# Performance work log

Hardware: AMD Instinct MI355X
Metric: run time of the kernel (lower is better)

The kernel has to match this reference:

```python
import jax, jax.numpy as jnp
import numpy as np
import math

CHANNELS = 1024
N_HEADS = 16
K_CHANNELS = CHANNELS // N_HEADS  # 64
ROPE_D = int(K_CHANNELS * 0.5)    # 32
B, T = 4, 2048


def apply_rope(x, d, base=10000.0):
    # x: [b, h, t, c]; rotate first d dims, pass the rest through
    t = x.shape[2]
    theta = 1.0 / (base ** (jnp.arange(0, d, 2, dtype=jnp.float32) / d))  # [d/2]
    idx_theta = jnp.arange(t, dtype=jnp.float32)[:, None] * theta[None, :]  # [t, d/2]
    idx_theta2 = jnp.concatenate([idx_theta, idx_theta], axis=-1)  # [t, d]
    cos = jnp.cos(idx_theta2)[None, None, :, :]
    sin = jnp.sin(idx_theta2)[None, None, :, :]
    x_rope, x_pass = x[..., :d], x[..., d:]
    d2 = d // 2
    neg_half = jnp.concatenate([-x_rope[..., d2:], x_rope[..., :d2]], axis=-1)
    x_rope = x_rope * cos + neg_half * sin
    return jnp.concatenate([x_rope, x_pass], axis=-1)


def setup_inputs() -> dict:
    key = jax.random.key(0)
    ks = jax.random.split(key, 12)
    xavier = math.sqrt(6.0 / (CHANNELS + CHANNELS))
    inp = {
        "x": jax.random.normal(ks[0], (B, CHANNELS, T), dtype=jnp.float32),
        "c": jax.random.normal(ks[1], (B, CHANNELS, T), dtype=jnp.float32),
        "attn_mask": jnp.ones((1, 1, T, T), dtype=jnp.int32),
        "wq": jax.random.uniform(ks[2], (CHANNELS, CHANNELS), jnp.float32, -xavier, xavier),
        "bq": jnp.zeros((CHANNELS,), jnp.float32),
        "wk": jax.random.uniform(ks[3], (CHANNELS, CHANNELS), jnp.float32, -xavier, xavier),
        "bk": jnp.zeros((CHANNELS,), jnp.float32),
        "wv": jax.random.uniform(ks[4], (CHANNELS, CHANNELS), jnp.float32, -xavier, xavier),
        "bv": jnp.zeros((CHANNELS,), jnp.float32),
        "wo": jax.random.normal(ks[5], (CHANNELS, CHANNELS), jnp.float32) * (1.0 / math.sqrt(CHANNELS)),
        "bo": jnp.zeros((CHANNELS,), jnp.float32),
    }
    return inp


def reference(x, c, attn_mask, wq, bq, wk, bk, wv, bv, wo, bo):
    b, _, t_t = x.shape
    t_s = c.shape[2]
    # Conv1d with kernel size 1 == per-timestep linear
    q = jnp.einsum('oi,bit->bot', wq, x) + bq[None, :, None]
    k = jnp.einsum('oi,bit->bot', wk, c) + bk[None, :, None]
    v = jnp.einsum('oi,bit->bot', wv, c) + bv[None, :, None]
    # b (h c) t -> b h t c
    def split_heads(z, t):
        return z.reshape(b, N_HEADS, K_CHANNELS, t).transpose(0, 1, 3, 2)
    q = split_heads(q, t_t)
    k = split_heads(k, t_s)
    v = split_heads(v, t_s)
    q = apply_rope(q, ROPE_D)
    k = apply_rope(k, ROPE_D)
    scores = jnp.einsum('bhqc,bhkc->bhqk', q, k) / math.sqrt(K_CHANNELS)
    scores = jnp.where(attn_mask == 0, jnp.float32(-10000.0), scores)
    p_attn = jax.nn.softmax(scores, axis=-1)
    out = jnp.einsum('bhqk,bhkc->bhqc', p_attn, v)
    # b h t c -> b h c t -> b (h c) t
    out = out.transpose(0, 1, 3, 2).reshape(b, CHANNELS, t_t)
    out = jnp.einsum('oi,bit->bot', wo, out) + bo[None, :, None]
    return out
```

## Files before the change

### kernel.cpp

```cpp
#include <hip/hip_runtime.h>
#include <stdint.h>

#define TT 2048
#define CC 1024
#define NHH 16
#define HD 64

using short8  = __attribute__((ext_vector_type(8))) short;
using short4v = __attribute__((ext_vector_type(4))) short;
using f32x4   = __attribute__((ext_vector_type(4))) float;
using ushort8 = __attribute__((ext_vector_type(8))) unsigned short;

typedef const __attribute__((address_space(1))) void* gptr_t;
typedef __attribute__((address_space(3))) void* lptr_t;

__device__ __forceinline__ unsigned short f2bf(float f){
  union { float f; unsigned int u; } v; v.f = f;
  unsigned int r = v.u + 0x7fffu + ((v.u >> 16) & 1u);
  return (unsigned short)(r >> 16);
}
__device__ __forceinline__ float bf2f(unsigned short u){
  union { unsigned int u; float f; } v; v.u = ((unsigned int)u) << 16;
  return v.f;
}
__device__ __forceinline__ uint32_t cvtpk_bf16(float lo, float hi){
  uint32_t r;
  asm("v_cvt_pk_bf16_f32 %0, %1, %2" : "=v"(r) : "v"(lo), "v"(hi));
  return r;
}
__device__ __forceinline__ float fexp2(float x){
#if __has_builtin(__builtin_amdgcn_exp2f)
  return __builtin_amdgcn_exp2f(x);
#else
  return exp2f(x);
#endif
}
__device__ __forceinline__ f32x4 mfma16x16x16bf16(short4v a, short4v b, f32x4 c){
#if __has_builtin(__builtin_amdgcn_mfma_f32_16x16x16bf16_1k)
  return __builtin_amdgcn_mfma_f32_16x16x16bf16_1k(a, b, c, 0, 0, 0);
#else
  asm("v_mfma_f32_16x16x16_bf16 %0, %1, %2, %0" : "+v"(c) : "v"(a), "v"(b));
  return c;
#endif
}

__global__ void wconv_kernel(const float* __restrict__ wq, const float* __restrict__ wk,
                             const float* __restrict__ wv, const float* __restrict__ wo,
                             unsigned short* __restrict__ W){
  int w = blockIdx.x >> 9;
  const float* s = (w==0)? wq : (w==1)? wk : (w==2)? wv : wo;
  size_t rem = ((size_t)(blockIdx.x & 511) * 256 + threadIdx.x) * 8;
  float4 a = *(const float4*)(s + rem);
  float4 b = *(const float4*)(s + rem + 4);
  ushort8 o;
  o[0]=f2bf(a.x); o[1]=f2bf(a.y); o[2]=f2bf(a.z); o[3]=f2bf(a.w);
  o[4]=f2bf(b.x); o[5]=f2bf(b.y); o[6]=f2bf(b.z); o[7]=f2bf(b.w);
  *(ushort8*)(W + (size_t)w*1048576 + rem) = o;
}

__global__ void tcast_kernel(const float* __restrict__ x, const float* __restrict__ c,
                             unsigned short* __restrict__ xT, unsigned short* __restrict__ cT){
  int z = blockIdx.z; int tensor = z >> 2; int b = z & 3;
  const float* src = (tensor ? c : x) + (size_t)b*CC*TT;
  unsigned short* dst = (tensor ? cT : xT) + (size_t)b*TT*CC;
  int t0 = blockIdx.x*64, c0 = blockIdx.y*64;
  __shared__ unsigned short ls[64][66];
  int tid = threadIdx.x;
  int r = tid >> 2, q = tid & 3;
  const float4* p = (const float4*)(src + (size_t)(c0+r)*TT + t0 + q*16);
  float4 vv[4]; vv[0]=p[0]; vv[1]=p[1]; vv[2]=p[2]; vv[3]=p[3];
  unsigned short* lp = &ls[r][q*16];
#pragma unroll
  for (int i=0;i<4;i++){
    lp[i*4+0]=f2bf(vv[i].x); lp[i*4+1]=f2bf(vv[i].y);
    lp[i*4+2]=f2bf(vv[i].z); lp[i*4+3]=f2bf(vv[i].w);
  }
  __syncthreads();
  unsigned short tmp[16] __attribute__((aligned(16)));
#pragma unroll
  for (int j=0;j<16;j++) tmp[j] = ls[q*16+j][r];
  unsigned short* dp = dst + (size_t)(t0+r)*CC + c0 + q*16;
  *(ushort8*)dp       = *(ushort8*)tmp;
  *(ushort8*)(dp + 8) = *(ushort8*)(tmp+8);
}

__device__ __forceinline__ void rope_write(
    const f32x4 (&acc)[4][4], const float* __restrict__ bias,
    unsigned short* __restrict__ dst,
    int b, int m0, int wr, int n0, int wc, int lane, float sc)
{
  int crow = (lane>>4)*4;
  int h = (m0 + wr) >> 6;
  size_t bh = (size_t)b*NHH + h;
  float th[4];
#pragma unroll
  for (int r=0;r<4;r++)
    th[r] = exp2f(-0.8304820237218405f * (float)(crow + r));
  float bv[4][4];
#pragma unroll
  for (int m=0;m<4;m++)
#pragma unroll
    for (int r=0;r<4;r++)
      bv[m][r] = bias[m0 + wr + m*16 + crow + r];
#pragma unroll
  for (int n=0;n<4;n++){
    int t = n0 + wc + n*16 + (lane&15);
    float tf = (float)t;
    float o_[4][4];
#pragma unroll
    for (int r=0;r<4;r++){
      float sn, cs;
      sincosf(tf * th[r], &sn, &cs);
      float v0 = acc[0][n][r] + bv[0][r];
      float v1 = acc[1][n][r] + bv[1][r];
      o_[0][r] = (v0*cs - v1*sn)*sc;
      o_[1][r] = (v1*cs + v0*sn)*sc;
      o_[2][r] = (acc[2][n][r] + bv[2][r])*sc;
      o_[3][r] = (acc[3][n][r] + bv[3][r])*sc;
    }
    unsigned short* dp = dst + (bh*TT + t)*HD + crow;
#pragma unroll
    for (int m=0;m<4;m++){
      uint2 pk;
      pk.x = cvtpk_bf16(o_[m][0], o_[m][1]);
      pk.y = cvtpk_bf16(o_[m][2], o_[m][3]);
      *(uint2*)(dp + m*16) = pk;
    }
  }
}

template<bool F32OUT>
__global__ __launch_bounds__(256) void gemm_kernel(
    const unsigned short* __restrict__ A,
    const unsigned short* __restrict__ Bm,
    const float* __restrict__ bias,
    void* __restrict__ outp)
{
  __shared__ unsigned short As[128*64];
  __shared__ unsigned short Bs[128*64];
  int b  = blockIdx.z;
  int m0 = blockIdx.x * 128;
  int n0 = blockIdx.y * 128;
  const unsigned short* Bb = Bm + (size_t)b*TT*CC;
  int tid = threadIdx.x;
  int lane = tid & 63, wave = tid >> 6;
  int wr = (wave>>1)*64, wc = (wave&1)*64;
  int srow = lane >> 3;
  int scolb = ((lane & 7) ^ srow) << 4;
  f32x4 acc[4][4] = {};
  for (int kt = 0; kt < 1024; kt += 64){
    __syncthreads();
#pragma unroll
    for (int i=0;i<4;i++){
      int ch = wave*4 + i;
      int row = ch*8 + srow;
      const char* g = (const char*)(A + (size_t)(m0+row)*1024 + kt) + scolb;
      __builtin_amdgcn_global_load_lds((gptr_t)g, (lptr_t)(As + ch*512), 16, 0, 0);
    }
#pragma unroll
    for (int i=0;i<4;i++){
      int ch = wave*4 + i;
      int row = ch*8 + srow;
      const char* g = (const char*)(Bb + (size_t)(n0+row)*1024 + kt) + scolb;
      __builtin_amdgcn_global_load_lds((gptr_t)g, (lptr_t)(Bs + ch*512), 16, 0, 0);
    }
    __syncthreads();
#pragma unroll
    for (int kk=0;kk<2;kk++){
      int kb = kk*64 + ((lane>>4)<<4);
      short8 af[4], bf[4];
#pragma unroll
      for (int m=0;m<4;m++){
        int row = wr + m*16 + (lane&15);
        af[m] = *(const short8*)((const char*)As + row*128 + (kb ^ ((row&7)<<4)));
      }
#pragma unroll
      for (int n=0;n<4;n++){
        int row = wc + n*16 + (lane&15);
        bf[n] = *(const short8*)((const char*)Bs + row*128 + (kb ^ ((row&7)<<4)));
      }
#pragma unroll
      for (int m=0;m<4;m++)
#pragma unroll
        for (int n=0;n<4;n++)
          acc[m][n] = __builtin_amdgcn_mfma_f32_16x16x32_bf16(af[m], bf[n], acc[m][n], 0, 0, 0);
    }
  }
  int crow = (lane>>4)*4;
#pragma unroll
  for (int m=0;m<4;m++){
#pragma unroll
    for (int r=0;r<4;r++){
      int o = m0 + wr + m*16 + crow + r;
      float bv = bias[o];
#pragma unroll
      for (int n=0;n<4;n++){
        int t = n0 + wc + n*16 + (lane&15);
        float v = acc[m][n][r] + bv;
        if (F32OUT) ((float*)outp)[(size_t)b*CC*TT + (size_t)o*TT + t] = v;
        else ((unsigned short*)outp)[(size_t)b*CC*TT + (size_t)o*TT + t] = f2bf(v);
      }
    }
  }
}

__global__ __launch_bounds__(256) void q_gemm_kernel(
    const unsigned short* __restrict__ A,
    const unsigned short* __restrict__ Bm,
    const float* __restrict__ bias,
    unsigned short* __restrict__ Qh)
{
  __shared__ unsigned short As[128*64];
  __shared__ unsigned short Bs[128*64];
  int b  = blockIdx.z;
  int m0 = blockIdx.x * 128;
  int n0 = blockIdx.y * 128;
  const unsigned short* Bb = Bm + (size_t)b*TT*CC;
  int tid = threadIdx.x;
  int lane = tid & 63, wave = tid >> 6;
  int wr = (wave>>1)*64, wc = (wave&1)*64;
  int srow = lane >> 3;
  int scolb = ((lane & 7) ^ srow) << 4;
  f32x4 acc[4][4] = {};
  for (int kt = 0; kt < 1024; kt += 64){
    __syncthreads();
#pragma unroll
    for (int i=0;i<4;i++){
      int ch = wave*4 + i;
      int row = ch*8 + srow;
      const char* g = (const char*)(A + (size_t)(m0+row)*1024 + kt) + scolb;
      __builtin_amdgcn_global_load_lds((gptr_t)g, (lptr_t)(As + ch*512), 16, 0, 0);
      const char* g2 = (const char*)(Bb + (size_t)(n0+row)*1024 + kt) + scolb;
      __builtin_amdgcn_global_load_lds((gptr_t)g2, (lptr_t)(Bs + ch*512), 16, 0, 0);
    }
    __syncthreads();
#pragma unroll
    for (int kk=0;kk<2;kk++){
      int kb = kk*64 + ((lane>>4)<<4);
      short8 af[4], bf[4];
#pragma unroll
      for (int m=0;m<4;m++){
        int row = wr + m*16 + (lane&15);
        af[m] = *(const short8*)((const char*)As + row*128 + (kb ^ ((row&7)<<4)));
      }
#pragma unroll
      for (int n=0;n<4;n++){
        int row = wc + n*16 + (lane&15);
        bf[n] = *(const short8*)((const char*)Bs + row*128 + (kb ^ ((row&7)<<4)));
      }
#pragma unroll
      for (int m=0;m<4;m++)
#pragma unroll
        for (int n=0;n<4;n++)
          acc[m][n] = __builtin_amdgcn_mfma_f32_16x16x32_bf16(af[m], bf[n], acc[m][n], 0, 0, 0);
    }
  }
  rope_write(acc, bias, Qh, b, m0, wr, n0, wc, lane, 0.18033688011112042f);
}

__global__ __launch_bounds__(256, 2) void kv_gemm_kernel(
    const unsigned short* __restrict__ Wk,
    const unsigned short* __restrict__ Wv,
    const unsigned short* __restrict__ Bm,
    const float* __restrict__ biask, const float* __restrict__ biasv,
    unsigned short* __restrict__ Kh, unsigned short* __restrict__ outV)
{
  __shared__ unsigned short AsK[128*64];
  __shared__ unsigned short AsV[128*64];
  __shared__ unsigned short Bs[128*64];
  int b  = blockIdx.z;
  int m0 = blockIdx.x * 128;
  int n0 = blockIdx.y * 128;
  const unsigned short* Bb = Bm + (size_t)b*TT*CC;
  int tid = threadIdx.x;
  int lane = tid & 63, wave = tid >> 6;
  int wr = (wave>>1)*64, wc = (wave&1)*64;
  int srow = lane >> 3;
  int scolb = ((lane & 7) ^ srow) << 4;
  f32x4 accK[4][4] = {};
  f32x4 accV[4][4] = {};
  for (int kt = 0; kt < 1024; kt += 64){
    __syncthreads();
#pragma unroll
    for (int i=0;i<4;i++){
      int ch = wave*4 + i;
      int row = ch*8 + srow;
      const char* gk = (const char*)(Wk + (size_t)(m0+row)*1024 + kt) + scolb;
      __builtin_amdgcn_global_load_lds((gptr_t)gk, (lptr_t)(AsK + ch*512), 16, 0, 0);
      const char* gv = (const char*)(Wv + (size_t)(m0+row)*1024 + kt) + scolb;
      __builtin_amdgcn_global_load_lds((gptr_t)gv, (lptr_t)(AsV + ch*512), 16, 0, 0);
      const char* gb = (const char*)(Bb + (size_t)(n0+row)*1024 + kt) + scolb;
      __builtin_amdgcn_global_load_lds((gptr_t)gb, (lptr_t)(Bs + ch*512), 16, 0, 0);
    }
    __syncthreads();
#pragma unroll
    for (int kk=0;kk<2;kk++){
      int kb = kk*64 + ((lane>>4)<<4);
      short8 bf[4];
#pragma unroll
      for (int n=0;n<4;n++){
        int row = wc + n*16 + (lane&15);
        bf[n] = *(const short8*)((const char*)Bs + row*128 + (kb ^ ((row&7)<<4)));
      }
#pragma unroll
      for (int m=0;m<4;m++){
        int row = wr + m*16 + (lane&15);
        int ro = row*128 + (kb ^ ((row&7)<<4));
        short8 afk = *(const short8*)((const char*)AsK + ro);
        short8 afv = *(const short8*)((const char*)AsV + ro);
#pragma unroll
        for (int n=0;n<4;n++){
          accK[m][n] = __builtin_amdgcn_mfma_f32_16x16x32_bf16(afk, bf[n], accK[m][n], 0, 0, 0);
          accV[m][n] = __builtin_amdgcn_mfma_f32_16x16x32_bf16(afv, bf[n], accV[m][n], 0, 0, 0);
        }
      }
    }
  }
  int crow = (lane>>4)*4;
#pragma unroll
  for (int m=0;m<4;m++){
#pragma unroll
    for (int r=0;r<4;r++){
      int o = m0 + wr + m*16 + crow + r;
      float bvv = biasv[o];
#pragma unroll
      for (int n=0;n<4;n++){
        int t = n0 + wc + n*16 + (lane&15);
        outV[(size_t)b*CC*TT + (size_t)o*TT + t] = f2bf(accV[m][n][r] + bvv);
      }
    }
  }
  rope_write(accK, biask, Kh, b, m0, wr, n0, wc, lane, 1.0f);
}

__global__ __launch_bounds__(256, 4) void attn_kernel(
    const unsigned short* __restrict__ Qh, const unsigned short* __restrict__ Kh,
    const unsigned short* __restrict__ Vn, unsigned short* __restrict__ AO)
{
  __shared__ unsigned short Ks[2][64*64];
  __shared__ unsigned short Vs[2][64*64];
  int Hf = blockIdx.x + (blockIdx.y << 4);
  int s8 = Hf >> 3;
  int bh = (Hf & 7) + ((s8 >> 4) << 3);
  int q0 = (s8 & 15) * 128;
  int b = bh >> 4, h = bh & 15;
  int tid = threadIdx.x, lane = tid & 63, wave = tid >> 6;
  const unsigned short* Qb = Qh + (size_t)bh*TT*HD;
  const unsigned short* Kb = Kh + (size_t)bh*TT*HD;
  const unsigned short* Vb = Vn + (size_t)b*CC*TT + (size_t)h*64*TT;
  int srow = lane >> 3, scolb = ((lane & 7) ^ srow) << 4;
  int g = lane >> 4;

  union { short4v s; uint32_t u[2]; } ones;
  ones.u[0] = ((lane & 15) == 0) ? 0x3F803F80u : 0u;
  ones.u[1] = ones.u[0];

  short8 qf[2][2];
#pragma unroll
  for (int n=0;n<2;n++)
#pragma unroll
    for (int kk=0;kk<2;kk++){
      int qrow = q0 + wave*32 + n*16 + (lane&15);
      qf[n][kk] = *(const short8*)((const char*)(Qb + (size_t)qrow*HD) + kk*64 + g*16);
    }

  f32x4 accO[4][2] = {};
  f32x4 accL[2] = {};

#pragma unroll
  for (int i=0;i<2;i++){
    int ch = wave*2 + i;
    int row = ch*8 + srow;
    const char* gk = (const char*)(Kb + (size_t)row*HD) + scolb;
    __builtin_amdgcn_global_load_lds((gptr_t)gk, (lptr_t)(Ks[0] + ch*512), 16, 0, 0);
    const char* gv = (const char*)(Vb + (size_t)row*TT) + scolb;
    __builtin_amdgcn_global_load_lds((gptr_t)gv, (lptr_t)(Vs[0] + ch*512), 16, 0, 0);
  }
  __syncthreads();

  const int NT = TT/64;
  for (int t=0; t<NT; ++t){
    int cur = t & 1;
    if (t+1 < NT){
      int kv0n = (t+1)*64;
#pragma unroll
      for (int i=0;i<2;i++){
        int ch = wave*2 + i;
        int row = ch*8 + srow;
        const char* gk = (const char*)(Kb + (size_t)(kv0n+row)*HD) + scolb;
        __builtin_amdgcn_global_load_lds((gptr_t)gk, (lptr_t)(Ks[cur^1] + ch*512), 16, 0, 0);
        const char* gv = (const char*)(Vb + (size_t)row*TT + kv0n) + scolb;
        __builtin_amdgcn_global_load_lds((gptr_t)gv, (lptr_t)(Vs[cur^1] + ch*512), 16, 0, 0);
      }
    }

    const char* KsC = (const char*)Ks[cur];
    f32x4 accS[4][2];
#pragma unroll
    for (int m=0;m<4;m++)
#pragma unroll
      for (int n=0;n<2;n++){
        accS[m][n][0]=accS[m][n][1]=accS[m][n][2]=accS[m][n][3]=-16.0f;
      }
    __builtin_amdgcn_s_setprio(1);
#pragma unroll
    for (int kk=0;kk<2;kk++){
      int kb = kk*64 + g*16;
      short8 kf[4];
#pragma unroll
      for (int m=0;m<4;m++){
        int row = m*16 + (lane&15);
        kf[m] = *(const short8*)(KsC + row*128 + (kb ^ ((row&7)<<4)));
      }
#pragma unroll
      for (int m=0;m<4;m++)
#pragma unroll
        for (int n=0;n<2;n++)
          accS[m][n] = __builtin_amdgcn_mfma_f32_16x16x32_bf16(kf[m], qf[n][kk], accS[m][n], 0, 0, 0);
    }
    __builtin_amdgcn_s_setprio(0);

#pragma unroll
    for (int n=0;n<2;n++)
#pragma unroll
      for (int m=0;m<4;m++)
#pragma unroll
        for (int r=0;r<4;r++)
          accS[m][n][r] = fexp2(accS[m][n][r]);

    union { short4v s; uint32_t u[2]; } pu[4][2];
#pragma unroll
    for (int m=0;m<4;m++)
#pragma unroll
      for (int n=0;n<2;n++){
        pu[m][n].u[0] = cvtpk_bf16(accS[m][n][0], accS[m][n][1]);
        pu[m][n].u[1] = cvtpk_bf16(accS[m][n][2], accS[m][n][3]);
      }
    const char* VsC = (const char*)Vs[cur];
    int r7 = lane & 7;
    int halfb = (g & 1) << 3;
    __builtin_amdgcn_s_setprio(1);
#pragma unroll
    for (int m=0;m<4;m++){
      int slot = m*2 + (g>>1);
      int coff = ((slot ^ r7) << 4) | halfb;
#pragma unroll
      for (int dt=0;dt<4;dt++){
        int row = dt*16 + (lane&15);
        short4v vf = *(const short4v*)(VsC + row*128 + coff);
#pragma unroll
        for (int n=0;n<2;n++)
          accO[dt][n] = mfma16x16x16bf16(vf, pu[m][n].s, accO[dt][n]);
      }
#pragma unroll
      for (int n=0;n<2;n++)
        accL[n] = mfma16x16x16bf16(ones.s, pu[m][n].s, accL[n]);
    }
    __builtin_amdgcn_s_setprio(0);

    __syncthreads();
  }

#pragma unroll
  for (int n=0;n<2;n++){
    int t = q0 + wave*32 + n*16 + (lane&15);
    float lsum = __shfl(accL[n][0], lane & 15);
    float rl = 1.0f / lsum;
#pragma unroll
    for (int m=0;m<4;m++){
      uint2 pk;
      pk.x = cvtpk_bf16(accO[m][n][0]*rl, accO[m][n][1]*rl);
      pk.y = cvtpk_bf16(accO[m][n][2]*rl, accO[m][n][3]*rl);
      *(uint2*)(AO + ((size_t)b*TT + t)*CC + h*64 + m*16 + g*4) = pk;
    }
  }
}

extern "C" void kernel_launch(void* const* d_in, const int* in_sizes, int n_in,
                              void* d_out, int out_size, void* d_ws, size_t ws_size,
                              hipStream_t stream) {
  const float* x  = (const float*)d_in[0];
  const float* c  = (const float*)d_in[1];
  const float* wq = (const float*)d_in[3];
  const float* bq = (const float*)d_in[4];
  const float* wk = (const float*)d_in[5];
  const float* bk = (const float*)d_in[6];
  const float* wv = (const float*)d_in[7];
  const float* bv = (const float*)d_in[8];
  const float* wo = (const float*)d_in[9];
  const float* bo = (const float*)d_in[10];

  unsigned short* W   = (unsigned short*)d_ws;
  unsigned short* xT  = W   + 4194304;
  unsigned short* cT  = xT  + 8388608;
  unsigned short* QKV = cT  + 8388608;
  unsigned short* Qh  = QKV + 25165824;
  unsigned short* Kh  = Qh  + 8388608;
  unsigned short* V   = QKV + 16777216;
  unsigned short* AO  = QKV;

  wconv_kernel<<<dim3(2048), dim3(256), 0, stream>>>(wq, wk, wv, wo, W);
  tcast_kernel<<<dim3(32,16,8), dim3(256), 0, stream>>>(x, c, xT, cT);
  q_gemm_kernel<<<dim3(8,16,4), dim3(256), 0, stream>>>(W, xT, bq, Qh);
  kv_gemm_kernel<<<dim3(8,16,4), dim3(256), 0, stream>>>(W + 1048576, W + 2097152, cT,
                                                         bk, bv, Kh, V);
  attn_kernel<<<dim3(16,64), dim3(256), 0, stream>>>(Qh, Kh, V, AO);
  gemm_kernel<true><<<dim3(8,16,4), dim3(256), 0, stream>>>(W + 3145728, AO, bo, d_out);
}
```

Measured before the change: 193.8 us.

## Split attention work across 8 waves with one 16-row query tile each

The attention kernel moves from 4 waves handling 32 query rows each to 8 waves (512 threads) handling 16 query rows each, so each wave keeps half the accumulators and issues half the MFMAs per KV tile. Each wave now loads one 8-row chunk of K and V into LDS instead of two. The aim is lower register pressure and more waves in flight to hide latency. In exchange, each K/V fragment read from LDS feeds only one query tile instead of two, which doubles LDS read traffic per FLOP, and barrier sync now spans more waves.

```diff
diff --git a/kernel.cpp b/kernel.cpp
--- a/kernel.cpp
+++ b/kernel.cpp
@@ -333,7 +333,7 @@
   rope_write(accK, biask, Kh, b, m0, wr, n0, wc, lane, 1.0f);
 }
 
-__global__ __launch_bounds__(256, 4) void attn_kernel(
+__global__ __launch_bounds__(512, 8) void attn_kernel(
     const unsigned short* __restrict__ Qh, const unsigned short* __restrict__ Kh,
     const unsigned short* __restrict__ Vn, unsigned short* __restrict__ AO)
 {
@@ -350,31 +350,29 @@
   const unsigned short* Vb = Vn + (size_t)b*CC*TT + (size_t)h*64*TT;
   int srow = lane >> 3, scolb = ((lane & 7) ^ srow) << 4;
   int g = lane >> 4;
+  int r7 = lane & 7;
+  int halfb = (g & 1) << 3;
 
   union { short4v s; uint32_t u[2]; } ones;
   ones.u[0] = ((lane & 15) == 0) ? 0x3F803F80u : 0u;
   ones.u[1] = ones.u[0];
 
-  short8 qf[2][2];
-#pragma unroll
-  for (int n=0;n<2;n++)
-#pragma unroll
-    for (int kk=0;kk<2;kk++){
-      int qrow = q0 + wave*32 + n*16 + (lane&15);
-      qf[n][kk] = *(const short8*)((const char*)(Qb + (size_t)qrow*HD) + kk*64 + g*16);
-    }
-
-  f32x4 accO[4][2] = {};
-  f32x4 accL[2] = {};
-
-#pragma unroll
-  for (int i=0;i<2;i++){
-    int ch = wave*2 + i;
-    int row = ch*8 + srow;
+  short8 qf[2];
+#pragma unroll
+  for (int kk=0;kk<2;kk++){
+    int qrow = q0 + wave*16 + (lane&15);
+    qf[kk] = *(const short8*)((const char*)(Qb + (size_t)qrow*HD) + kk*64 + g*16);
+  }
+
+  f32x4 accO[4] = {};
+  f32x4 accL = {};
+
+  {
+    int row = wave*8 + srow;
     const char* gk = (const char*)(Kb + (size_t)row*HD) + scolb;
-    __builtin_amdgcn_global_load_lds((gptr_t)gk, (lptr_t)(Ks[0] + ch*512), 16, 0, 0);
+    __builtin_amdgcn_global_load_lds((gptr_t)gk, (lptr_t)(Ks[0] + wave*512), 16, 0, 0);
     const char* gv = (const char*)(Vb + (size_t)row*TT) + scolb;
-    __builtin_amdgcn_global_load_lds((gptr_t)gv, (lptr_t)(Vs[0] + ch*512), 16, 0, 0);
+    __builtin_amdgcn_global_load_lds((gptr_t)gv, (lptr_t)(Vs[0] + wave*512), 16, 0, 0);
   }
   __syncthreads();
 
@@ -383,62 +381,45 @@
     int cur = t & 1;
     if (t+1 < NT){
       int kv0n = (t+1)*64;
-#pragma unroll
-      for (int i=0;i<2;i++){
-        int ch = wave*2 + i;
-        int row = ch*8 + srow;
-        const char* gk = (const char*)(Kb + (size_t)(kv0n+row)*HD) + scolb;
-        __builtin_amdgcn_global_load_lds((gptr_t)gk, (lptr_t)(Ks[cur^1] + ch*512), 16, 0, 0);
-        const char* gv = (const char*)(Vb + (size_t)row*TT + kv0n) + scolb;
-        __builtin_amdgcn_global_load_lds((gptr_t)gv, (lptr_t)(Vs[cur^1] + ch*512), 16, 0, 0);
-      }
+      int row = wave*8 + srow;
+      const char* gk = (const char*)(Kb + (size_t)(kv0n+row)*HD) + scolb;
+      __builtin_amdgcn_global_load_lds((gptr_t)gk, (lptr_t)(Ks[cur^1] + wave*512), 16, 0, 0);
+      const char* gv = (const char*)(Vb + (size_t)row*TT + kv0n) + scolb;
+      __builtin_amdgcn_global_load_lds((gptr_t)gv, (lptr_t)(Vs[cur^1] + wave*512), 16, 0, 0);
     }
 
     const char* KsC = (const char*)Ks[cur];
-    f32x4 accS[4][2];
-#pragma unroll
-    for (int m=0;m<4;m++)
-#pragma unroll
-      for (int n=0;n<2;n++){
-        accS[m][n][0]=accS[m][n][1]=accS[m][n][2]=accS[m][n][3]=-16.0f;
-      }
+    f32x4 accS[4];
+#pragma unroll
+    for (int m=0;m<4;m++){
+      accS[m][0]=accS[m][1]=accS[m][2]=accS[m][3]=-16.0f;
+    }
     __builtin_amdgcn_s_setprio(1);
 #pragma unroll
     for (int kk=0;kk<2;kk++){
       int kb = kk*64 + g*16;
-      short8 kf[4];
 #pragma unroll
       for (int m=0;m<4;m++){
         int row = m*16 + (lane&15);
-        kf[m] = *(const short8*)(KsC + row*128 + (kb ^ ((row&7)<<4)));
-      }
-#pragma unroll
-      for (int m=0;m<4;m++)
-#pragma unroll
-        for (int n=0;n<2;n++)
-          accS[m][n] = __builtin_amdgcn_mfma_f32_16x16x32_bf16(kf[m], qf[n][kk], accS[m][n], 0, 0, 0);
+        short8 kf = *(const short8*)(KsC + row*128 + (kb ^ ((row&7)<<4)));
+        accS[m] = __builtin_amdgcn_mfma_f32_16x16x32_bf16(kf, qf[kk], accS[m], 0, 0, 0);
+      }
     }
     __builtin_amdgcn_s_setprio(0);
 
 #pragma unroll
-    for (int n=0;n<2;n++)
-#pragma unroll
-      for (int m=0;m<4;m++)
-#pragma unroll
-        for (int r=0;r<4;r++)
-          accS[m][n][r] = fexp2(accS[m][n][r]);
-
-    union { short4v s; uint32_t u[2]; } pu[4][2];
-#pragma unroll
     for (int m=0;m<4;m++)
 #pragma unroll
-      for (int n=0;n<2;n++){
-        pu[m][n].u[0] = cvtpk_bf16(accS[m][n][0], accS[m][n][1]);
-        pu[m][n].u[1] = cvtpk_bf16(accS[m][n][2], accS[m][n][3]);
-      }
+      for (int r=0;r<4;r++)
+        accS[m][r] = fexp2(accS[m][r]);
+
+    union { short4v s; uint32_t u[2]; } pu[4];
+#pragma unroll
+    for (int m=0;m<4;m++){
+      pu[m].u[0] = cvtpk_bf16(accS[m][0], accS[m][1]);
+      pu[m].u[1] = cvtpk_bf16(accS[m][2], accS[m][3]);
+    }
     const char* VsC = (const char*)Vs[cur];
-    int r7 = lane & 7;
-    int halfb = (g & 1) << 3;
     __builtin_amdgcn_s_setprio(1);
 #pragma unroll
     for (int m=0;m<4;m++){
@@ -448,29 +429,24 @@
       for (int dt=0;dt<4;dt++){
         int row = dt*16 + (lane&15);
         short4v vf = *(const short4v*)(VsC + row*128 + coff);
-#pragma unroll
-        for (int n=0;n<2;n++)
-          accO[dt][n] = mfma16x16x16bf16(vf, pu[m][n].s, accO[dt][n]);
-      }
-#pragma unroll
-      for (int n=0;n<2;n++)
-        accL[n] = mfma16x16x16bf16(ones.s, pu[m][n].s, accL[n]);
+        accO[dt] = mfma16x16x16bf16(vf, pu[m].s, accO[dt]);
+      }
+      accL = mfma16x16x16bf16(ones.s, pu[m].s, accL);
     }
     __builtin_amdgcn_s_setprio(0);
 
     __syncthreads();
   }
 
-#pragma unroll
-  for (int n=0;n<2;n++){
-    int t = q0 + wave*32 + n*16 + (lane&15);
-    float lsum = __shfl(accL[n][0], lane & 15);
+  {
+    int t = q0 + wave*16 + (lane&15);
+    float lsum = __shfl(accL[0], lane & 15);
     float rl = 1.0f / lsum;
 #pragma unroll
     for (int m=0;m<4;m++){
       uint2 pk;
-      pk.x = cvtpk_bf16(accO[m][n][0]*rl, accO[m][n][1]*rl);
-      pk.y = cvtpk_bf16(accO[m][n][2]*rl, accO[m][n][3]*rl);
+      pk.x = cvtpk_bf16(accO[m][0]*rl, accO[m][1]*rl);
+      pk.y = cvtpk_bf16(accO[m][2]*rl, accO[m][3]*rl);
       *(uint2*)(AO + ((size_t)b*TT + t)*CC + h*64 + m*16 + g*4) = pk;
     }
   }
@@ -504,6 +480,6 @@
   q_gemm_kernel<<<dim3(8,16,4), dim3(256), 0, stream>>>(W, xT, bq, Qh);
   kv_gemm_kernel<<<dim3(8,16,4), dim3(256), 0, stream>>>(W + 1048576, W + 2097152, cT,
                                                          bk, bv, Kh, V);
-  attn_kernel<<<dim3(16,64), dim3(256), 0, stream>>>(Qh, Kh, V, AO);
+  attn_kernel<<<dim3(16,64), dim3(512), 0, stream>>>(Qh, Kh, V, AO);
   gemm_kernel<true><<<dim3(8,16,4), dim3(256), 0, stream>>>(W + 3145728, AO, bo, d_out);
 }
```

Result: slower. 215.7 us (+11.3%).
